# Performance work log

Hardware: AMD Instinct MI355X
Metric: run time of the kernel (lower is better)

## Reference

```python
import jax, jax.numpy as jnp
import numpy as np
import math

B, L, D = 2, 2048, 1024
H, HD = 16, 64          # num heads, head dim
R = 256                 # kv lora rank = D // 4
E, K, F = 8, 2, 1024    # routed experts, top_k, intermediate size


def rmsnorm(x, w, eps=1e-6):
    ms = jnp.mean(x * x, axis=-1, keepdims=True)
    return w * (x * jax.lax.rsqrt(ms + eps))


def setup_inputs() -> dict:
    key = jax.random.key(0)
    ks = jax.random.split(key, 16)
    s = 0.02
    return {
        "x": jax.random.normal(ks[0], (B, L, D), jnp.float32),
        "ln1_w": jnp.ones((D,), jnp.float32),
        "q_w": jax.random.normal(ks[1], (D, H * HD), jnp.float32) * s,
        "kvd_w": jax.random.normal(ks[2], (D, R), jnp.float32) * s,
        "kvn_w": jnp.ones((R,), jnp.float32),
        "kvu_w": jax.random.normal(ks[3], (R, 2 * H * HD), jnp.float32) * s,
        "o_w": jax.random.normal(ks[4], (H * HD, D), jnp.float32) * s,
        "ln2_w": jnp.ones((D,), jnp.float32),
        "gate_w": jax.random.normal(ks[5], (D, E), jnp.float32) * s,
        "sh_w1": jax.random.normal(ks[6], (D, F), jnp.float32) * s,
        "sh_w2": jax.random.normal(ks[7], (F, D), jnp.float32) * s,
        "sh_w3": jax.random.normal(ks[8], (D, F), jnp.float32) * s,
        "re_w1": jax.random.normal(ks[9], (E, D, F), jnp.float32) * s,
        "re_w2": jax.random.normal(ks[10], (E, F, D), jnp.float32) * s,
        "re_w3": jax.random.normal(ks[11], (E, D, F), jnp.float32) * s,
    }


def reference(x, ln1_w, q_w, kvd_w, kvn_w, kvu_w, o_w, ln2_w, gate_w,
              sh_w1, sh_w2, sh_w3, re_w1, re_w2, re_w3):
    # ---- MLHA attention with pre-RMSNorm and latent-compressed KV ----
    xn = rmsnorm(x, ln1_w)
    q = (xn @ q_w).reshape(B, L, H, HD)
    latent = rmsnorm(xn @ kvd_w, kvn_w)                 # [B,L,R]
    kv = latent @ kvu_w                                 # [B,L,2*H*HD]
    k, v = jnp.split(kv, 2, axis=-1)
    k = k.reshape(B, L, H, HD)
    v = v.reshape(B, L, H, HD)
    scores = jnp.einsum('bxhd,byhd->bhxy', q, k) / math.sqrt(HD)
    causal = jnp.tril(jnp.ones((L, L), bool))
    scores = jnp.where(causal, scores, -jnp.inf)
    attn = jax.nn.softmax(scores, axis=-1)
    attn_out = jnp.einsum('bhxy,byhd->bxhd', attn, v).reshape(B, L, H * HD)
    h = x + attn_out @ o_w

    # ---- MoE (inference: no jitter, expert_bias = 0, no bias update) ----
    hn = rmsnorm(h, ln2_w)
    flat = hn.reshape(-1, D)                            # [T,D], T=B*L
    # shared expert (SwiGLU)
    shared = (jax.nn.silu(flat @ sh_w1) * (flat @ sh_w3)) @ sh_w2
    # router
    logits = flat @ gate_w                              # [T,E]
    probs = jax.nn.softmax(logits, axis=-1)
    topw, topi = jax.lax.top_k(probs, K)                # [T,K]
    topw = topw / jnp.sum(topw, axis=-1, keepdims=True)
    # per-token per-expert combine weight [T,E]
    combine = jnp.sum(topw[..., None] * jax.nn.one_hot(topi, E, dtype=flat.dtype), axis=1)
    # all routed experts densely, then masked combine (same math as masked loop)
    h1 = jnp.einsum('td,edf->etf', flat, re_w1)
    h3 = jnp.einsum('td,edf->etf', flat, re_w3)
    eo = jnp.einsum('etf,efd->etd', jax.nn.silu(h1) * h3, re_w2)
    routed = jnp.einsum('te,etd->td', combine, eo)
    moe_out = (shared + routed).reshape(B, L, D)
    return h + moe_out, probs
```

## Files before the change

kernel.cpp:

```cpp
#include <hip/hip_runtime.h>
#include <hip/hip_bf16.h>
#include <cstdint>
#include <cstddef>

typedef unsigned short u16;
typedef unsigned int u32;
typedef __attribute__((ext_vector_type(8))) short bf16x8;
typedef __attribute__((ext_vector_type(4))) float f32x4;

static constexpr int Bb = 2, Ll = 2048, Dd = 1024, Hh = 16, Rr = 256, Ee = 8, Ff = 1024;
static constexpr int Tt = Bb * Ll;

__device__ __forceinline__ u16 f2bf(float f){
  union { float f; u32 u; } v; v.f = f;
  u32 u = v.u;
  u32 r = u + 0x7FFFu + ((u >> 16) & 1u);
  return (u16)(r >> 16);
}
__device__ __forceinline__ float bf2f(u16 b){
  union { u32 u; float f; } v; v.u = ((u32)b) << 16; return v.f;
}

#define GLDS(gp, lp) __builtin_amdgcn_global_load_lds( \
    (const __attribute__((address_space(1))) unsigned int*)(gp), \
    (__attribute__((address_space(3))) unsigned int*)(lp), 16, 0, 0)

__global__ void transpose5(const float* __restrict__ q_w, const float* __restrict__ o_w,
                           const float* __restrict__ w1, const float* __restrict__ w3,
                           const float* __restrict__ w2,
                           u16* __restrict__ qkvdT, u16* __restrict__ oT,
                           u16* __restrict__ sh13T, u16* __restrict__ sh2T){
  const float* s; u16* d; int off, str;
  switch (blockIdx.z){
    case 0: s = q_w; d = qkvdT; off = 0; str = 1; break;
    case 1: s = o_w; d = oT;    off = 0; str = 1; break;
    case 2: s = w1;  d = sh13T; off = 0; str = 2; break;
    case 3: s = w3;  d = sh13T; off = 1; str = 2; break;
    default: s = w2; d = sh2T;  off = 0; str = 1; break;
  }
  __shared__ float tile[32][33];
  int bx = blockIdx.x * 32, by = blockIdx.y * 32;
  int tx = threadIdx.x, ty = threadIdx.y;
  #pragma unroll
  for (int i = ty; i < 32; i += 8) tile[i][tx] = s[(size_t)(by + i) * 1024 + bx + tx];
  __syncthreads();
  #pragma unroll
  for (int i = ty; i < 32; i += 8)
    d[(size_t)(off + (bx + i) * str) * 1024 + by + tx] = f2bf(tile[tx][i]);
}

__global__ void transposeEx(const float* __restrict__ re_w1, const float* __restrict__ re_w3,
                            const float* __restrict__ re_w2,
                            u16* __restrict__ re13T, u16* __restrict__ re2T){
  int z = blockIdx.z, which = z >> 3, e = z & 7;
  const float* s; u16* d; int off, str;
  size_t eo = (size_t)e * 1024 * 1024;
  if (which == 0){ s = re_w1 + eo; d = re13T + (size_t)e * 2048 * 1024; off = 0; str = 2; }
  else if (which == 1){ s = re_w3 + eo; d = re13T + (size_t)e * 2048 * 1024; off = 1; str = 2; }
  else { s = re_w2 + eo; d = re2T + (size_t)e * 1024 * 1024; off = 0; str = 1; }
  __shared__ float tile[32][33];
  int bx = blockIdx.x * 32, by = blockIdx.y * 32;
  int tx = threadIdx.x, ty = threadIdx.y;
  #pragma unroll
  for (int i = ty; i < 32; i += 8) tile[i][tx] = s[(size_t)(by + i) * 1024 + bx + tx];
  __syncthreads();
  #pragma unroll
  for (int i = ty; i < 32; i += 8)
    d[(size_t)(off + (bx + i) * str) * 1024 + by + tx] = f2bf(tile[tx][i]);
}

__global__ void transpose_conv(const float* __restrict__ src, u16* __restrict__ dst,
                               int K, int N, int dstOff){
  __shared__ float tile[32][33];
  int bx = blockIdx.x * 32, by = blockIdx.y * 32;
  int tx = threadIdx.x, ty = threadIdx.y;
  #pragma unroll
  for (int i = ty; i < 32; i += 8) tile[i][tx] = src[(size_t)(by + i) * N + bx + tx];
  __syncthreads();
  #pragma unroll
  for (int i = ty; i < 32; i += 8)
    dst[(size_t)(dstOff + bx + i) * K + by + tx] = f2bf(tile[tx][i]);
}

template<int DIM>
__global__ void rmsnorm_kernel(const float* __restrict__ x, const float* __restrict__ w,
                               u16* __restrict__ out){
  int t = blockIdx.x;
  const float* xr = x + (size_t)t * DIM;
  u16* orow = out + (size_t)t * DIM;
  int tid = threadIdx.x;
  constexpr int NT = 256;
  constexpr int PER = DIM / NT > 0 ? DIM / NT : 1;
  float vals[PER];
  float ss = 0.f;
  #pragma unroll
  for (int i = 0; i < PER; i++){
    int d = tid + i * NT;
    float v = (d < DIM) ? xr[d] : 0.f;
    vals[i] = v; ss += v * v;
  }
  __shared__ float red[4];
  for (int m = 32; m; m >>= 1) ss += __shfl_xor(ss, m, 64);
  if ((tid & 63) == 0) red[tid >> 6] = ss;
  __syncthreads();
  float tot = red[0] + red[1] + red[2] + red[3];
  float rn = rsqrtf(tot / DIM + 1e-6f);
  #pragma unroll
  for (int i = 0; i < PER; i++){
    int d = tid + i * NT;
    if (d < DIM) orow[d] = f2bf(vals[i] * rn * w[d]);
  }
}

__global__ void router_kernel(const float* __restrict__ h, const float* __restrict__ ln2w,
                              const float* __restrict__ gate,
                              float* __restrict__ probs_out,
                              int* __restrict__ topi, float* __restrict__ topw,
                              u16* __restrict__ hn){
  int t = blockIdx.x; int tid = threadIdx.x;
  const float* hr = h + (size_t)t * Dd;
  float v[4]; float ss = 0.f;
  #pragma unroll
  for (int i = 0; i < 4; i++){ float x = hr[tid + i * 256]; v[i] = x; ss += x * x; }
  __shared__ float red[4];
  for (int m = 32; m; m >>= 1) ss += __shfl_xor(ss, m, 64);
  if ((tid & 63) == 0) red[tid >> 6] = ss;
  __syncthreads();
  float rn = rsqrtf((red[0] + red[1] + red[2] + red[3]) / Dd + 1e-6f);
  float p[8];
  #pragma unroll
  for (int e = 0; e < 8; e++) p[e] = 0.f;
  #pragma unroll
  for (int i = 0; i < 4; i++){
    int d = tid + i * 256;
    float hv = v[i] * rn * ln2w[d];
    hn[(size_t)t * Dd + d] = f2bf(hv);
    const float* g = gate + (size_t)d * 8;
    #pragma unroll
    for (int e = 0; e < 8; e++) p[e] += hv * g[e];
  }
  #pragma unroll
  for (int e = 0; e < 8; e++){
    float x = p[e];
    for (int m = 32; m; m >>= 1) x += __shfl_xor(x, m, 64);
    p[e] = x;
  }
  __shared__ float pe[4][8];
  if ((tid & 63) == 0){ for (int e = 0; e < 8; e++) pe[tid >> 6][e] = p[e]; }
  __syncthreads();
  if (tid == 0){
    float lg[8];
    for (int e = 0; e < 8; e++) lg[e] = pe[0][e] + pe[1][e] + pe[2][e] + pe[3][e];
    float mx = lg[0];
    for (int e = 1; e < 8; e++) mx = fmaxf(mx, lg[e]);
    float pr[8]; float s = 0.f;
    for (int e = 0; e < 8; e++){ pr[e] = __expf(lg[e] - mx); s += pr[e]; }
    float inv = 1.f / s;
    for (int e = 0; e < 8; e++) probs_out[(size_t)t * 8 + e] = pr[e] * inv;
    int i0 = 0;
    for (int e = 1; e < 8; e++) if (pr[e] > pr[i0]) i0 = e;
    int i1 = -1;
    for (int e = 0; e < 8; e++){ if (e == i0) continue; if (i1 < 0 || pr[e] > pr[i1]) i1 = e; }
    float w0 = pr[i0], w1 = pr[i1]; float wn = 1.f / (w0 + w1);
    topi[t * 2] = i0; topi[t * 2 + 1] = i1;
    topw[t * 2] = w0 * wn; topw[t * 2 + 1] = w1 * wn;
  }
}

__global__ void hist_kernel(const int* __restrict__ topi, int* __restrict__ counts){
  __shared__ int h[8];
  int tid = threadIdx.x;
  if (tid < 8) h[tid] = 0;
  __syncthreads();
  int base = blockIdx.x * 512;
  for (int i = tid; i < 512; i += 256) atomicAdd(&h[topi[base + i]], 1);
  __syncthreads();
  if (tid < 8) atomicAdd(&counts[tid], h[tid]);
}

__global__ void bucket_kernel(const int* __restrict__ topi, const float* __restrict__ topw,
                              const int* __restrict__ counts, int* __restrict__ cur,
                              int* __restrict__ entries, float* __restrict__ ew){
  __shared__ int lh[8], lbase[8], lcur[8], loffs[8];
  int tid = threadIdx.x;
  if (tid < 8) lh[tid] = 0;
  __syncthreads();
  int t = blockIdx.x * 256 + tid;
  int e0 = topi[t * 2], e1 = topi[t * 2 + 1];
  atomicAdd(&lh[e0], 1); atomicAdd(&lh[e1], 1);
  __syncthreads();
  if (tid == 0){
    int c = 0;
    for (int e = 0; e < 8; e++){ loffs[e] = c; c += counts[e]; }
  }
  if (tid < 8){ lbase[tid] = atomicAdd(&cur[tid], lh[tid]); lcur[tid] = 0; }
  __syncthreads();
  int p0 = atomicAdd(&lcur[e0], 1);
  int pos0 = loffs[e0] + lbase[e0] + p0;
  entries[pos0] = t; ew[pos0] = topw[t * 2];
  int p1 = atomicAdd(&lcur[e1], 1);
  int pos1 = loffs[e1] + lbase[e1] + p1;
  entries[pos1] = t; ew[pos1] = topw[t * 2 + 1];
}

template<int TM, int ROWMODE, int MODE>
__launch_bounds__(256)
__global__ void gemm_bt(const u16* __restrict__ A, const u16* __restrict__ Bt,
                        void* __restrict__ C, const float* __restrict__ res,
                        int M, int N, int K, int lda, int ldc,
                        const int* __restrict__ entries, const float* __restrict__ ew,
                        const int* __restrict__ counts,
                        float* __restrict__ outAt){
  constexpr int MTC = TM / 32;
  __shared__ __align__(16) u16 As[TM * 32];
  __shared__ __align__(16) u16 Bs[128 * 32];
  __shared__ int els[TM];
  __shared__ float ewl[TM];

  int e = (ROWMODE ? blockIdx.z : 0);
  const u16* Bte = Bt + (size_t)e * N * K;
  int cnt, off;
  if (ROWMODE == 0){ cnt = M; off = 0; }
  else {
    cnt = counts[e];
    off = 0;
    for (int i = 0; i < e; i++) off += counts[i];
  }
  int rt = blockIdx.y * TM;
  if (rt >= cnt) return;
  int cb = blockIdx.x * 128;
  int tid = threadIdx.x;

  if (ROWMODE >= 1){
    if (tid < TM){
      int r = rt + tid;
      els[tid] = (r < cnt) ? entries[off + r] : 0;
      ewl[tid] = (MODE == 4 && r < cnt) ? ew[off + r] : 0.f;
    }
    __syncthreads();
  }

  int sr = tid >> 2;
  int skc = (tid & 3) * 8;
  int rr0 = rt + sr, rr1 = rt + sr + 64;
  size_t ar0 = 0, ar1 = 0;
  if (ROWMODE == 0){ ar0 = (size_t)rr0; ar1 = (size_t)rr1; }
  else if (ROWMODE == 1){ ar0 = (size_t)els[sr];
                          ar1 = (TM == 128) ? (size_t)els[sr + 64] : 0; }
  else {
    int c0 = rr0 < cnt ? rr0 : (cnt - 1);
    int c1 = rr1 < cnt ? rr1 : (cnt - 1);
    ar0 = (size_t)off + c0; ar1 = (size_t)off + c1;
  }
  const u16* pa0 = A + ar0 * lda + skc;
  const u16* pa1 = A + ar1 * lda + skc;
  const u16* pb0 = Bte + (size_t)(cb + sr) * K + skc;
  const u16* pb1 = Bte + (size_t)(cb + sr + 64) * K + skc;
  u16* lA0 = &As[tid * 8];
  u16* lA1 = &As[(TM == 128 ? 2048 : 0) + tid * 8];
  u16* lB0 = &Bs[tid * 8];
  u16* lB1 = &Bs[2048 + tid * 8];

  int w = tid >> 6, lane = tid & 63;
  int wm = w >> 1, wn = w & 1;
  int quad = lane >> 4, l16 = lane & 15;

  f32x4 acc[MTC][4];
  const f32x4 zf = {0.f, 0.f, 0.f, 0.f};
  #pragma unroll
  for (int i = 0; i < MTC; i++)
    #pragma unroll
    for (int j = 0; j < 4; j++) acc[i][j] = zf;

  for (int k0 = 0; k0 < K; k0 += 32){
    __syncthreads();
    GLDS(pa0 + k0, lA0);
    if (TM == 128) GLDS(pa1 + k0, lA1);
    GLDS(pb0 + k0, lB0);
    GLDS(pb1 + k0, lB1);
    __syncthreads();
    bf16x8 af[MTC], bfr[4];
    #pragma unroll
    for (int mt = 0; mt < MTC; mt++)
      af[mt] = *(const bf16x8*)&As[(wm * (TM / 2) + mt * 16 + l16) * 32 + quad * 8];
    #pragma unroll
    for (int nt = 0; nt < 4; nt++)
      bfr[nt] = *(const bf16x8*)&Bs[(wn * 64 + nt * 16 + l16) * 32 + quad * 8];
    #pragma unroll
    for (int mt = 0; mt < MTC; mt++)
      #pragma unroll
      for (int nt = 0; nt < 4; nt++)
        acc[mt][nt] = __builtin_amdgcn_mfma_f32_16x16x32_bf16(af[mt], bfr[nt], acc[mt][nt], 0, 0, 0);
  }

  #pragma unroll
  for (int mt = 0; mt < MTC; mt++){
    #pragma unroll
    for (int nt = 0; nt < 4; nt++){
      #pragma unroll
      for (int r = 0; r < 4; r++){
        int row = wm * (TM / 2) + mt * 16 + quad * 4 + r;
        int col = cb + wn * 64 + nt * 16 + l16;
        int rr = rt + row;
        float v = acc[mt][nt][r];
        if (MODE == 6){
          float pv = __shfl_xor(v, 1, 64);
          if (rr < cnt && (l16 & 1) == 0){
            float sl = v / (1.f + __expf(-v));
            size_t crow = (size_t)((ROWMODE == 1) ? (off + rr) : rr);
            ((u16*)C)[crow * ldc + (col >> 1)] = f2bf(sl * pv);
          }
          continue;
        }
        if (rr >= cnt) continue;
        if (MODE == 0){
          size_t ci = (size_t)((ROWMODE == 1) ? (off + rr) : rr) * ldc + col;
          ((u16*)C)[ci] = f2bf(v);
        } else if (MODE == 1){
          size_t ci = (size_t)rr * ldc + col;
          ((float*)C)[ci] = v + res[ci];
        } else if (MODE == 5){
          if (col < 1024) ((u16*)C)[(size_t)rr * 1024 + col] = f2bf(v);
          else            outAt[(size_t)rr * 256 + (col - 1024)] = v;
        } else {
          int tok = els[row];
          atomicAdd(&outAt[(size_t)tok * ldc + col], ewl[row] * v);
        }
      }
    }
  }
}

__global__ void vt_kernel(const u16* __restrict__ kv, u16* __restrict__ vt){
  __shared__ __align__(16) u16 t[64 * 72];
  int kt = blockIdx.x * 64, h = blockIdx.y, b = blockIdx.z;
  size_t bL = (size_t)b * Ll;
  int tid = threadIdx.x;
  int r = tid >> 2, c0 = (tid & 3) * 16;
  const u16* src = kv + (bL + kt + r) * 2048 + 1024 + h * 64 + c0;
  *(uint4*)&t[r * 72 + c0]     = *(const uint4*)(src);
  *(uint4*)&t[r * 72 + c0 + 8] = *(const uint4*)(src + 8);
  __syncthreads();
  int d = tid >> 2; int k0 = (tid & 3) * 16;
  u16 tmp[16];
  #pragma unroll
  for (int j = 0; j < 16; j++) tmp[j] = t[(k0 + j) * 72 + d];
  u16* dst = vt + ((size_t)(b * Hh + h) * 64 + d) * (size_t)Ll + kt + k0;
  *(uint4*)dst       = *(const uint4*)&tmp[0];
  *(uint4*)(dst + 8) = *(const uint4*)&tmp[8];
}

__launch_bounds__(256)
__global__ void attn_kernel(const u16* __restrict__ q, const u16* __restrict__ kv,
                            const u16* __restrict__ vt, u16* __restrict__ out){
  constexpr int LD = 72;
  const float CS = 0.18033688011112042f;
  __shared__ __align__(16) u16 Ks[64 * LD];
  __shared__ __align__(16) u16 Vs[64 * LD];
  __shared__ __align__(16) u16 Ps[64 * LD];
  int h = blockIdx.y, b = blockIdx.z;
  size_t bL = (size_t)b * Ll;
  int tid = threadIdx.x, w = tid >> 6, lane = tid & 63, quad = lane >> 4, l16 = lane & 15;
  int sr = tid >> 2, sc = (tid & 3) * 16;
  const u16* kbase = kv + (bL + sr) * 2048 + h * 64 + sc;
  const u16* vbase = vt + ((size_t)(b * Hh + h) * 64 + sr) * (size_t)Ll + sc;
  const f32x4 zf = {0.f, 0.f, 0.f, 0.f};

  #pragma unroll
  for (int pass = 0; pass < 2; pass++){
    int q0 = (pass ? (31 - (int)blockIdx.x) : (int)blockIdx.x) * 64;
    int qrow = q0 + w * 16 + l16;

    bf16x8 qf[2];
    #pragma unroll
    for (int ks = 0; ks < 2; ks++)
      qf[ks] = *(const bf16x8*)(q + (bL + qrow) * 1024 + h * 64 + ks * 32 + quad * 8);

    f32x4 oacc[4];
    #pragma unroll
    for (int dt = 0; dt < 4; dt++) oacc[dt] = zf;
    float mprev = -1e30f, lsum = 0.f;

    for (int kt = 0; kt <= q0; kt += 64){
      __syncthreads();
      {
        const u16* kp = kbase + (size_t)kt * 2048;
        *(uint4*)&Ks[sr * LD + sc]     = *(const uint4*)(kp);
        *(uint4*)&Ks[sr * LD + sc + 8] = *(const uint4*)(kp + 8);
        const u16* vp = vbase + kt;
        *(uint4*)&Vs[sr * LD + sc]     = *(const uint4*)(vp);
        *(uint4*)&Vs[sr * LD + sc + 8] = *(const uint4*)(vp + 8);
      }
      __syncthreads();

      f32x4 sacc[4];
      #pragma unroll
      for (int mt = 0; mt < 4; mt++) sacc[mt] = zf;
      #pragma unroll
      for (int ks = 0; ks < 2; ks++){
        #pragma unroll
        for (int mt = 0; mt < 4; mt++){
          bf16x8 kf = *(const bf16x8*)&Ks[(mt * 16 + l16) * LD + ks * 32 + quad * 8];
          sacc[mt] = __builtin_amdgcn_mfma_f32_16x16x32_bf16(kf, qf[ks], sacc[mt], 0, 0, 0);
        }
      }
      bool diag = (kt == q0);
      int lq = w * 16 + l16;
      float sv[16]; float mx = -1e30f;
      #pragma unroll
      for (int mt = 0; mt < 4; mt++){
        #pragma unroll
        for (int r = 0; r < 4; r++){
          float s = sacc[mt][r] * CS;
          if (diag && (mt * 16 + quad * 4 + r > lq)) s = -1e30f;
          sv[mt * 4 + r] = s;
          mx = fmaxf(mx, s);
        }
      }
      mx = fmaxf(mx, __shfl_xor(mx, 16, 64));
      mx = fmaxf(mx, __shfl_xor(mx, 32, 64));
      float mnew = fmaxf(mprev, mx);
      float alpha = exp2f(mprev - mnew);
      mprev = mnew;
      float rs = 0.f;
      #pragma unroll
      for (int mt = 0; mt < 4; mt++){
        float p0 = exp2f(sv[mt * 4 + 0] - mnew);
        float p1 = exp2f(sv[mt * 4 + 1] - mnew);
        float p2 = exp2f(sv[mt * 4 + 2] - mnew);
        float p3 = exp2f(sv[mt * 4 + 3] - mnew);
        rs += p0 + p1 + p2 + p3;
        union { uint2 u; __hip_bfloat162 h2[2]; } pk;
        pk.h2[0] = __float22bfloat162_rn(make_float2(p0, p1));
        pk.h2[1] = __float22bfloat162_rn(make_float2(p2, p3));
        *(uint2*)&Ps[(w * 16 + l16) * LD + mt * 16 + quad * 4] = pk.u;
      }
      rs += __shfl_xor(rs, 16, 64);
      rs += __shfl_xor(rs, 32, 64);
      lsum = lsum * alpha + rs;
      #pragma unroll
      for (int dt = 0; dt < 4; dt++) oacc[dt] *= alpha;

      #pragma unroll
      for (int ks = 0; ks < 2; ks++){
        bf16x8 pf = *(const bf16x8*)&Ps[(w * 16 + l16) * LD + ks * 32 + quad * 8];
        #pragma unroll
        for (int dt = 0; dt < 4; dt++){
          bf16x8 vf = *(const bf16x8*)&Vs[(dt * 16 + l16) * LD + ks * 32 + quad * 8];
          oacc[dt] = __builtin_amdgcn_mfma_f32_16x16x32_bf16(vf, pf, oacc[dt], 0, 0, 0);
        }
      }
    }

    float inv = 1.f / lsum;
    #pragma unroll
    for (int dt = 0; dt < 4; dt++){
      union { uint2 u; __hip_bfloat162 h2[2]; } ov;
      ov.h2[0] = __float22bfloat162_rn(make_float2(oacc[dt][0] * inv, oacc[dt][1] * inv));
      ov.h2[1] = __float22bfloat162_rn(make_float2(oacc[dt][2] * inv, oacc[dt][3] * inv));
      *(uint2*)(out + (bL + qrow) * 1024 + h * 64 + dt * 16 + quad * 4) = ov.u;
    }
  }
}

extern "C" void kernel_launch(void* const* d_in, const int* in_sizes, int n_in,
                              void* d_out, int out_size, void* d_ws, size_t ws_size,
                              hipStream_t stream){
  const float* x     = (const float*)d_in[0];
  const float* ln1_w = (const float*)d_in[1];
  const float* q_w   = (const float*)d_in[2];
  const float* kvd_w = (const float*)d_in[3];
  const float* kvn_w = (const float*)d_in[4];
  const float* kvu_w = (const float*)d_in[5];
  const float* o_w   = (const float*)d_in[6];
  const float* ln2_w = (const float*)d_in[7];
  const float* gate_w= (const float*)d_in[8];
  const float* sh_w1 = (const float*)d_in[9];
  const float* sh_w2 = (const float*)d_in[10];
  const float* sh_w3 = (const float*)d_in[11];
  const float* re_w1 = (const float*)d_in[12];
  const float* re_w2 = (const float*)d_in[13];
  const float* re_w3 = (const float*)d_in[14];
  float* out = (float*)d_out;

  char* wp = (char*)d_ws;
  auto alloc = [&](size_t bytes)->char*{
    char* p = wp; wp += (bytes + 255) & ~(size_t)255; return p;
  };
  u16* qkvdT = (u16*)alloc((size_t)1280 * 1024 * 2);
  u16* kvuT  = (u16*)alloc((size_t)2048 * 256 * 2);
  u16* oT    = (u16*)alloc((size_t)1024 * 1024 * 2);
  u16* sh13T = (u16*)alloc((size_t)2048 * 1024 * 2);
  u16* sh2T  = (u16*)alloc((size_t)1024 * 1024 * 2);
  u16* re13T = (u16*)alloc((size_t)8 * 2048 * 1024 * 2);
  u16* re2T  = (u16*)alloc((size_t)8 * 1024 * 1024 * 2);
  u16* xn    = (u16*)alloc((size_t)Tt * 1024 * 2);
  u16* qbuf  = (u16*)alloc((size_t)Tt * 1024 * 2);
  float* latpre = (float*)alloc((size_t)Tt * 256 * 4);
  u16* lat   = (u16*)alloc((size_t)Tt * 256 * 2);
  u16* kvbuf = (u16*)alloc((size_t)Tt * 2048 * 2);
  u16* attnb = (u16*)alloc((size_t)Tt * 1024 * 2);
  float* hbuf = (float*)alloc((size_t)Tt * 1024 * 4);
  u16* vtb   = (u16*)alloc((size_t)Bb * Hh * 64 * Ll * 2);
  u16* gr    = (u16*)alloc((size_t)Tt * 2 * 1024 * 2);
  int* counts = (int*)alloc(32);
  int* cur    = (int*)alloc(32);
  int* topi   = (int*)alloc((size_t)Tt * 2 * 4);
  float* topw = (float*)alloc((size_t)Tt * 2 * 4);
  int* entries= (int*)alloc((size_t)Tt * 2 * 4);
  float* ewt  = (float*)alloc((size_t)Tt * 2 * 4);
  (void)ws_size; (void)n_in; (void)in_sizes; (void)out_size;

  hipMemsetAsync(counts, 0, 32, stream);
  hipMemsetAsync(cur, 0, 32, stream);

  dim3 tb(32, 8);
  transpose5<<<dim3(32, 32, 5), tb, 0, stream>>>(q_w, o_w, sh_w1, sh_w3, sh_w2,
                                                 qkvdT, oT, sh13T, sh2T);
  transpose_conv<<<dim3(8, 32, 1), tb, 0, stream>>>(kvd_w, qkvdT, 1024, 256, 1024);
  transpose_conv<<<dim3(64, 8, 1), tb, 0, stream>>>(kvu_w, kvuT, 256, 2048, 0);
  transposeEx<<<dim3(32, 32, 24), tb, 0, stream>>>(re_w1, re_w3, re_w2, re13T, re2T);

  rmsnorm_kernel<1024><<<Tt, 256, 0, stream>>>(x, ln1_w, xn);

  gemm_bt<64,0,5><<<dim3(10, 64), 256, 0, stream>>>(xn, qkvdT, qbuf, nullptr,
      Tt, 1280, 1024, 1024, 1024, nullptr, nullptr, nullptr, latpre);
  rmsnorm_kernel<256><<<Tt, 256, 0, stream>>>(latpre, kvn_w, lat);
  gemm_bt<128,0,0><<<dim3(16, 32), 256, 0, stream>>>(lat, kvuT, kvbuf, nullptr,
      Tt, 2048, 256, 256, 2048, nullptr, nullptr, nullptr, nullptr);
  vt_kernel<<<dim3(32, 16, 2), 256, 0, stream>>>(kvbuf, vtb);
  attn_kernel<<<dim3(16, 16, 2), 256, 0, stream>>>(qbuf, kvbuf, vtb, attnb);
  gemm_bt<64,0,1><<<dim3(8, 64), 256, 0, stream>>>(attnb, oT, hbuf, x,
      Tt, 1024, 1024, 1024, 1024, nullptr, nullptr, nullptr, nullptr);
  router_kernel<<<Tt, 256, 0, stream>>>(hbuf, ln2_w, gate_w, out + (size_t)Tt * Dd,
                                        topi, topw, xn);
  hist_kernel<<<16, 256, 0, stream>>>(topi, counts);
  bucket_kernel<<<16, 256, 0, stream>>>(topi, topw, counts, cur, entries, ewt);

  gemm_bt<128,0,6><<<dim3(16, 32), 256, 0, stream>>>(xn, sh13T, kvbuf, nullptr,
      Tt, 2048, 1024, 1024, 1024, nullptr, nullptr, nullptr, nullptr);
  gemm_bt<64,0,1><<<dim3(8, 64), 256, 0, stream>>>(kvbuf, sh2T, out, hbuf,
      Tt, 1024, 1024, 1024, 1024, nullptr, nullptr, nullptr, nullptr);

  gemm_bt<128,1,6><<<dim3(16, 32, 8), 256, 0, stream>>>(xn, re13T, gr, nullptr,
      Tt, 2048, 1024, 1024, 1024, entries, nullptr, counts, nullptr);
  gemm_bt<128,2,4><<<dim3(8, 32, 8), 256, 0, stream>>>(gr, re2T, nullptr, nullptr,
      Tt, 1024, 1024, 1024, 1024, entries, ewt, counts, out);
}
```

Baseline: 577.4 us.

## Double-buffer K/V tiles in attention with register prefetch and lazy rescale

The attention loop now prefetches the next K and V tiles into registers while the current tile is computed, and stores them into a second shared-memory buffer, which cuts one barrier per iteration. The softmax scale is folded into the Q projection epilogue, so the per-score multiply is gone. The running-max rescale of the accumulators is skipped when no lane's max increased. MFMA sections are wrapped in s_setprio. The cost is more LDS and registers, which may lower occupancy, and scaling Q before bf16 rounding changes numerics slightly.

```diff
diff --git a/kernel.cpp b/kernel.cpp
--- a/kernel.cpp
+++ b/kernel.cpp
@@ -10,6 +10,7 @@
 
 static constexpr int Bb = 2, Ll = 2048, Dd = 1024, Hh = 16, Rr = 256, Ee = 8, Ff = 1024;
 static constexpr int Tt = Bb * Ll;
+static constexpr float QSCALE = 0.18033688011112042f;
 
 __device__ __forceinline__ u16 f2bf(float f){
   union { float f; u32 u; } v; v.f = f;
@@ -320,7 +321,7 @@
           size_t ci = (size_t)rr * ldc + col;
           ((float*)C)[ci] = v + res[ci];
         } else if (MODE == 5){
-          if (col < 1024) ((u16*)C)[(size_t)rr * 1024 + col] = f2bf(v);
+          if (col < 1024) ((u16*)C)[(size_t)rr * 1024 + col] = f2bf(v * QSCALE);
           else            outAt[(size_t)rr * 256 + (col - 1024)] = v;
         } else {
           int tok = els[row];
@@ -354,9 +355,8 @@
 __global__ void attn_kernel(const u16* __restrict__ q, const u16* __restrict__ kv,
                             const u16* __restrict__ vt, u16* __restrict__ out){
   constexpr int LD = 72;
-  const float CS = 0.18033688011112042f;
-  __shared__ __align__(16) u16 Ks[64 * LD];
-  __shared__ __align__(16) u16 Vs[64 * LD];
+  __shared__ __align__(16) u16 Ks[2][64 * LD];
+  __shared__ __align__(16) u16 Vs[2][64 * LD];
   __shared__ __align__(16) u16 Ps[64 * LD];
   int h = blockIdx.y, b = blockIdx.z;
   size_t bL = (size_t)b * Ll;
@@ -381,29 +381,44 @@
     for (int dt = 0; dt < 4; dt++) oacc[dt] = zf;
     float mprev = -1e30f, lsum = 0.f;
 
+    uint4 kr0 = *(const uint4*)(kbase);
+    uint4 kr1 = *(const uint4*)(kbase + 8);
+    uint4 vr0 = *(const uint4*)(vbase);
+    uint4 vr1 = *(const uint4*)(vbase + 8);
+    *(uint4*)&Ks[0][sr * LD + sc]     = kr0;
+    *(uint4*)&Ks[0][sr * LD + sc + 8] = kr1;
+    *(uint4*)&Vs[0][sr * LD + sc]     = vr0;
+    *(uint4*)&Vs[0][sr * LD + sc + 8] = vr1;
+    int cur = 0;
+    __syncthreads();
+
     for (int kt = 0; kt <= q0; kt += 64){
-      __syncthreads();
-      {
-        const u16* kp = kbase + (size_t)kt * 2048;
-        *(uint4*)&Ks[sr * LD + sc]     = *(const uint4*)(kp);
-        *(uint4*)&Ks[sr * LD + sc + 8] = *(const uint4*)(kp + 8);
-        const u16* vp = vbase + kt;
-        *(uint4*)&Vs[sr * LD + sc]     = *(const uint4*)(vp);
-        *(uint4*)&Vs[sr * LD + sc + 8] = *(const uint4*)(vp + 8);
-      }
-      __syncthreads();
+      bool pfetch = (kt + 64 <= q0);
+      if (pfetch){
+        const u16* kp = kbase + (size_t)(kt + 64) * 2048;
+        kr0 = *(const uint4*)(kp);
+        kr1 = *(const uint4*)(kp + 8);
+        const u16* vp = vbase + kt + 64;
+        vr0 = *(const uint4*)(vp);
+        vr1 = *(const uint4*)(vp + 8);
+      }
+      const u16* ksp = Ks[cur];
+      const u16* vsp = Vs[cur];
 
       f32x4 sacc[4];
       #pragma unroll
       for (int mt = 0; mt < 4; mt++) sacc[mt] = zf;
+      __builtin_amdgcn_s_setprio(1);
       #pragma unroll
       for (int ks = 0; ks < 2; ks++){
         #pragma unroll
         for (int mt = 0; mt < 4; mt++){
-          bf16x8 kf = *(const bf16x8*)&Ks[(mt * 16 + l16) * LD + ks * 32 + quad * 8];
+          bf16x8 kf = *(const bf16x8*)&ksp[(mt * 16 + l16) * LD + ks * 32 + quad * 8];
           sacc[mt] = __builtin_amdgcn_mfma_f32_16x16x32_bf16(kf, qf[ks], sacc[mt], 0, 0, 0);
         }
       }
+      __builtin_amdgcn_s_setprio(0);
+
       bool diag = (kt == q0);
       int lq = w * 16 + l16;
       float sv[16]; float mx = -1e30f;
@@ -411,7 +426,7 @@
       for (int mt = 0; mt < 4; mt++){
         #pragma unroll
         for (int r = 0; r < 4; r++){
-          float s = sacc[mt][r] * CS;
+          float s = sacc[mt][r];
           if (diag && (mt * 16 + quad * 4 + r > lq)) s = -1e30f;
           sv[mt * 4 + r] = s;
           mx = fmaxf(mx, s);
@@ -419,16 +434,21 @@
       }
       mx = fmaxf(mx, __shfl_xor(mx, 16, 64));
       mx = fmaxf(mx, __shfl_xor(mx, 32, 64));
-      float mnew = fmaxf(mprev, mx);
-      float alpha = exp2f(mprev - mnew);
-      mprev = mnew;
+      if (!__all(mx <= mprev)){
+        float mnew = fmaxf(mprev, mx);
+        float alpha = exp2f(mprev - mnew);
+        mprev = mnew;
+        lsum *= alpha;
+        #pragma unroll
+        for (int dt = 0; dt < 4; dt++) oacc[dt] *= alpha;
+      }
       float rs = 0.f;
       #pragma unroll
       for (int mt = 0; mt < 4; mt++){
-        float p0 = exp2f(sv[mt * 4 + 0] - mnew);
-        float p1 = exp2f(sv[mt * 4 + 1] - mnew);
-        float p2 = exp2f(sv[mt * 4 + 2] - mnew);
-        float p3 = exp2f(sv[mt * 4 + 3] - mnew);
+        float p0 = exp2f(sv[mt * 4 + 0] - mprev);
+        float p1 = exp2f(sv[mt * 4 + 1] - mprev);
+        float p2 = exp2f(sv[mt * 4 + 2] - mprev);
+        float p3 = exp2f(sv[mt * 4 + 3] - mprev);
         rs += p0 + p1 + p2 + p3;
         union { uint2 u; __hip_bfloat162 h2[2]; } pk;
         pk.h2[0] = __float22bfloat162_rn(make_float2(p0, p1));
@@ -437,19 +457,29 @@
       }
       rs += __shfl_xor(rs, 16, 64);
       rs += __shfl_xor(rs, 32, 64);
-      lsum = lsum * alpha + rs;
-      #pragma unroll
-      for (int dt = 0; dt < 4; dt++) oacc[dt] *= alpha;
-
+      lsum += rs;
+
+      __builtin_amdgcn_s_setprio(1);
       #pragma unroll
       for (int ks = 0; ks < 2; ks++){
-        bf16x8 pf = *(const bf16x8*)&Ps[(w * 16 + l16) * LD + ks * 32 + quad * 8];
+        bf16x8 pfr = *(const bf16x8*)&Ps[(w * 16 + l16) * LD + ks * 32 + quad * 8];
         #pragma unroll
         for (int dt = 0; dt < 4; dt++){
-          bf16x8 vf = *(const bf16x8*)&Vs[(dt * 16 + l16) * LD + ks * 32 + quad * 8];
-          oacc[dt] = __builtin_amdgcn_mfma_f32_16x16x32_bf16(vf, pf, oacc[dt], 0, 0, 0);
+          bf16x8 vf = *(const bf16x8*)&vsp[(dt * 16 + l16) * LD + ks * 32 + quad * 8];
+          oacc[dt] = __builtin_amdgcn_mfma_f32_16x16x32_bf16(vf, pfr, oacc[dt], 0, 0, 0);
         }
       }
+      __builtin_amdgcn_s_setprio(0);
+
+      if (pfetch){
+        int nb = cur ^ 1;
+        *(uint4*)&Ks[nb][sr * LD + sc]     = kr0;
+        *(uint4*)&Ks[nb][sr * LD + sc + 8] = kr1;
+        *(uint4*)&Vs[nb][sr * LD + sc]     = vr0;
+        *(uint4*)&Vs[nb][sr * LD + sc + 8] = vr1;
+        cur = nb;
+      }
+      __syncthreads();
     }
 
     float inv = 1.f / lsum;
```

New measurement: 560.2 us. 1.03x faster.
